# Kernel tuning notes

Measured on AMD Instinct MI355X. Metric: run time of the kernel, lower is better.

## Reference

```python
import jax, jax.numpy as jnp
import numpy as np
from jax.scipy.special import logsumexp

N = 4096
TAU = 2.0
IT = 30


def setup_inputs() -> dict:
    key = jax.random.key(0)
    k1, k2 = jax.random.split(key)
    eps = jax.random.normal(k1, (N, N), dtype=jnp.float32)
    mean = jax.random.uniform(k2, (N, N), dtype=jnp.float32)
    std = 10.0 * jnp.ones((N, N), dtype=jnp.float32)  # matches nn.Parameter(10*ones)
    return {"eps": eps, "mean": mean, "std": std}


def reference(eps, mean, std):
    # P_noisy = mean + std * eps ; Sinkhorn-Knopp in log domain, then exp.
    A = (mean + std * eps) / TAU

    def step(A, _):
        A = A - logsumexp(A, axis=1, keepdims=True)  # row normalize (log domain)
        A = A - logsumexp(A, axis=0, keepdims=True)  # col normalize (log domain)
        return A, None

    A, _ = jax.lax.scan(step, A, None, length=IT)
    return jnp.exp(A)
```

## Files before the change

kernel.cpp:

```cpp
#include <hip/hip_runtime.h>


constexpr int N    = 4096;
constexpr int IT   = 30;
constexpr int NBLK = 256;
constexpr int ROWS = 16;
constexpr int TPB  = 512;

typedef __attribute__((ext_vector_type(8))) unsigned short ushort8v;

__device__ inline float bf2f(unsigned int h) {
    union { unsigned int u; float f; } x; x.u = h << 16; return x.f;
}
__device__ inline unsigned short f2bf(float f) {
    union { float f; unsigned int u; } x; x.f = f;
    unsigned int r = x.u + 0x7FFFu + ((x.u >> 16) & 1u);
    return (unsigned short)(r >> 16);
}

struct V8 { float v[8]; };
struct V4 { float v[4]; };

template<typename PT> struct StoreOf;
template<> struct StoreOf<unsigned short> { using T = ushort8v; };
template<> struct StoreOf<float>          { using T = V8;       };

__device__ inline V8 unpackP(const ushort8v& s) {
    V8 r;
    #pragma unroll
    for (int k = 0; k < 8; ++k) r.v[k] = bf2f((unsigned int)s[k]);
    return r;
}
__device__ inline V8 unpackP(const V8& s) { return s; }

typedef __attribute__((ext_vector_type(4))) unsigned short ushort4v;
template<typename PT>
__device__ inline V4 loadP4(const PT* base, size_t e);
template<> __device__ inline V4 loadP4<unsigned short>(const unsigned short* base, size_t e) {
    ushort4v p = *(const ushort4v*)(base + e);
    V4 r;
    #pragma unroll
    for (int k = 0; k < 4; ++k) r.v[k] = bf2f((unsigned int)p[k]);
    return r;
}
template<> __device__ inline V4 loadP4<float>(const float* base, size_t e) {
    float4 a = *(const float4*)(base + e);
    V4 r = {{a.x, a.y, a.z, a.w}};
    return r;
}

template<typename PT>
__global__ __launch_bounds__(TPB) void k_first(const float* __restrict__ eps,
                                               const float* __restrict__ mean,
                                               const float* __restrict__ stdv,
                                               PT* __restrict__ P,
                                               float* __restrict__ partial,
                                               float* __restrict__ u_glob) {
    __shared__ float ldsRow[ROWS][8];
    __shared__ float ldsU[ROWS];
    const int t    = threadIdx.x;
    const int wv   = t >> 6, lane = t & 63;
    const int b    = blockIdx.x;
    const int col0 = t * 8;
    const int q    = t * 4;
    const int row0 = b * ROWS;

    typename StoreOf<PT>::T raw[ROWS];

    #pragma unroll
    for (int i = 0; i < ROWS; ++i) {
        const size_t rb = (size_t)(row0 + i) * N + col0;
        float4 e0 = *(const float4*)&eps [rb], e1 = *(const float4*)&eps [rb + 4];
        float4 m0 = *(const float4*)&mean[rb], m1 = *(const float4*)&mean[rb + 4];
        float4 s0 = *(const float4*)&stdv[rb], s1 = *(const float4*)&stdv[rb + 4];
        float p[8];
        p[0] = __expf((m0.x + s0.x * e0.x) * 0.5f);
        p[1] = __expf((m0.y + s0.y * e0.y) * 0.5f);
        p[2] = __expf((m0.z + s0.z * e0.z) * 0.5f);
        p[3] = __expf((m0.w + s0.w * e0.w) * 0.5f);
        p[4] = __expf((m1.x + s1.x * e1.x) * 0.5f);
        p[5] = __expf((m1.y + s1.y * e1.y) * 0.5f);
        p[6] = __expf((m1.z + s1.z * e1.z) * 0.5f);
        p[7] = __expf((m1.w + s1.w * e1.w) * 0.5f);
        if constexpr (sizeof(PT) == 2) {
            ushort8v o;
            #pragma unroll
            for (int k = 0; k < 8; ++k) o[k] = f2bf(p[k]);
            raw[i] = o;
            *(ushort8v*)((unsigned short*)P + rb) = o;
        } else {
            V8 r = {{p[0], p[1], p[2], p[3], p[4], p[5], p[6], p[7]}};
            raw[i] = r;
            float4 a = {p[0], p[1], p[2], p[3]}, bb = {p[4], p[5], p[6], p[7]};
            *(float4*)((float*)P + rb)     = a;
            *(float4*)((float*)P + rb + 4) = bb;
        }
    }

    #pragma unroll
    for (int i = 0; i < ROWS; ++i) {
        V8 pf = unpackP(raw[i]);
        float s = pf.v[0] + pf.v[1] + pf.v[2] + pf.v[3]
                + pf.v[4] + pf.v[5] + pf.v[6] + pf.v[7];
        #pragma unroll
        for (int off = 32; off; off >>= 1) s += __shfl_xor(s, off, 64);
        if (lane == 0) ldsRow[i][wv] = s;
    }
    __syncthreads();

    if (t < 8 * ROWS) {
        const int row = t >> 3, w = t & 7;
        float s = ldsRow[row][w];
        s += __shfl_xor(s, 1, 64);
        s += __shfl_xor(s, 2, 64);
        s += __shfl_xor(s, 4, 64);
        if (w == 0) {
            float u = __builtin_amdgcn_rcpf(s);
            ldsU[row] = u;
            u_glob[row0 + row] = u;
        }
    }
    __syncthreads();

    float acc[8] = {0, 0, 0, 0, 0, 0, 0, 0};
    #pragma unroll
    for (int i = 0; i < ROWS; ++i) {
        const float u = ldsU[i];
        V8 pf = unpackP(raw[i]);
        #pragma unroll
        for (int k = 0; k < 8; ++k) acc[k] += u * pf.v[k];
    }
    float4 a  = {acc[0], acc[1], acc[2], acc[3]};
    float4 bb = {acc[4], acc[5], acc[6], acc[7]};
    *(float4*)&partial[(size_t)b * N + q]        = a;
    *(float4*)&partial[(size_t)b * N + 2048 + q] = bb;
}

template<typename PT>
__global__ __launch_bounds__(TPB) void k_iter(const PT* __restrict__ P,
                                              const float* __restrict__ csum_prev,
                                              float* __restrict__ partial,
                                              float* __restrict__ u_glob) {
    __shared__ float ldsRow[ROWS][8];
    __shared__ float ldsU[ROWS];
    const int t    = threadIdx.x;
    const int wv   = t >> 6, lane = t & 63;
    const int b    = blockIdx.x;
    const int col0 = t * 8;
    const int q    = t * 4;
    const int row0 = b * ROWS;

    float4 c0 = *(const float4*)&csum_prev[q];
    float4 c1 = *(const float4*)&csum_prev[2048 + q];
    float v[8];
    v[0] = __builtin_amdgcn_rcpf(c0.x);  v[1] = __builtin_amdgcn_rcpf(c0.y);
    v[2] = __builtin_amdgcn_rcpf(c0.z);  v[3] = __builtin_amdgcn_rcpf(c0.w);
    v[4] = __builtin_amdgcn_rcpf(c1.x);  v[5] = __builtin_amdgcn_rcpf(c1.y);
    v[6] = __builtin_amdgcn_rcpf(c1.z);  v[7] = __builtin_amdgcn_rcpf(c1.w);

    typename StoreOf<PT>::T raw[ROWS];
    #pragma unroll
    for (int i = 0; i < ROWS; ++i)
        raw[i] = *(const typename StoreOf<PT>::T*)(P + (size_t)(row0 + i) * N + col0);

    #pragma unroll
    for (int i = 0; i < ROWS; ++i) {
        V8 pf = unpackP(raw[i]);
        float s = pf.v[0] * v[0] + pf.v[1] * v[1] + pf.v[2] * v[2] + pf.v[3] * v[3]
                + pf.v[4] * v[4] + pf.v[5] * v[5] + pf.v[6] * v[6] + pf.v[7] * v[7];
        #pragma unroll
        for (int off = 32; off; off >>= 1) s += __shfl_xor(s, off, 64);
        if (lane == 0) ldsRow[i][wv] = s;
    }
    __syncthreads();

    if (t < 8 * ROWS) {
        const int row = t >> 3, w = t & 7;
        float s = ldsRow[row][w];
        s += __shfl_xor(s, 1, 64);
        s += __shfl_xor(s, 2, 64);
        s += __shfl_xor(s, 4, 64);
        if (w == 0) {
            float u = __builtin_amdgcn_rcpf(s);
            ldsU[row] = u;
            u_glob[row0 + row] = u;
        }
    }
    __syncthreads();

    float acc[8] = {0, 0, 0, 0, 0, 0, 0, 0};
    #pragma unroll
    for (int i = 0; i < ROWS; ++i) {
        const float u = ldsU[i];
        V8 pf = unpackP(raw[i]);
        #pragma unroll
        for (int k = 0; k < 8; ++k) acc[k] += u * pf.v[k];
    }
    float4 a  = {acc[0], acc[1], acc[2], acc[3]};
    float4 bb = {acc[4], acc[5], acc[6], acc[7]};
    *(float4*)&partial[(size_t)b * N + q]        = a;
    *(float4*)&partial[(size_t)b * N + 2048 + q] = bb;
}

__global__ __launch_bounds__(512) void k_reduce(const float* __restrict__ partial,
                                                float* __restrict__ csum_cur) {
    __shared__ float red[16][32];
    const int t = threadIdx.x;
    const int lane = t & 63, wv = t >> 6;
    const int c     = blockIdx.x * 32 + (lane & 31);
    const int slice = wv * 2 + (lane >> 5);
    const float* p = partial + (size_t)(slice * 16) * N + c;
    float s = 0.0f;
    #pragma unroll 16
    for (int r = 0; r < 16; ++r)
        s += p[(size_t)r * N];
    red[slice][lane & 31] = s;
    __syncthreads();
    if (t < 32) {
        float acc = 0.0f;
        #pragma unroll
        for (int sl = 0; sl < 16; ++sl) acc += red[sl][t];
        csum_cur[blockIdx.x * 32 + t] = acc;
    }
}

template<typename PT>
__global__ __launch_bounds__(256) void k_final(const PT* __restrict__ P,
                                               const float* __restrict__ u_glob,
                                               const float* __restrict__ csum_last,
                                               float* __restrict__ out) {
    const int idx = blockIdx.x * 256 + threadIdx.x;
    const int row = idx >> 10;
    const int c4  = (idx & 1023) * 4;
    const float u = u_glob[row];
    const int perm = ((c4 & 4) ? 2048 : 0) + ((c4 >> 3) << 2);
    float4 cc = *(const float4*)&csum_last[perm];
    V4 p = loadP4(P, (size_t)row * N + c4);
    float4 r;
    r.x = p.v[0] * u * __builtin_amdgcn_rcpf(cc.x);
    r.y = p.v[1] * u * __builtin_amdgcn_rcpf(cc.y);
    r.z = p.v[2] * u * __builtin_amdgcn_rcpf(cc.z);
    r.w = p.v[3] * u * __builtin_amdgcn_rcpf(cc.w);
    ((float4*)out)[(size_t)idx] = r;
}

extern "C" void kernel_launch(void* const* d_in, const int* in_sizes, int n_in,
                              void* d_out, int out_size, void* d_ws, size_t ws_size,
                              hipStream_t stream) {
    const float* eps  = (const float*)d_in[0];
    const float* mean = (const float*)d_in[1];
    const float* stdv = (const float*)d_in[2];
    float* out = (float*)d_out;
    char* ws = (char*)d_ws;

    float* bufA   = (float*)ws;
    float* bufB   = bufA + N;
    float* u_glob = bufB + N;
    const size_t partOff = 64 * 1024;
    float* partial = (float*)(ws + partOff);
    const size_t partBytes = (size_t)NBLK * N * sizeof(float);
    const size_t pOff   = partOff + partBytes;
    const size_t pBytes = (size_t)N * N * sizeof(unsigned short);

    const int finalGrid = N * N / 4 / 256;

    float* cs[2] = { bufA, bufB };

    if (ws_size >= pOff + pBytes) {
        unsigned short* P = (unsigned short*)(ws + pOff);
        k_first<unsigned short><<<NBLK, TPB, 0, stream>>>(eps, mean, stdv, P, partial, u_glob);
        k_reduce<<<128, 512, 0, stream>>>(partial, cs[1]);
        for (int t = 2; t <= IT; ++t) {
            k_iter<unsigned short><<<NBLK, TPB, 0, stream>>>(P, cs[(t - 1) & 1], partial, u_glob);
            k_reduce<<<128, 512, 0, stream>>>(partial, cs[t & 1]);
        }
        k_final<unsigned short><<<finalGrid, 256, 0, stream>>>(P, u_glob, cs[IT & 1], out);
    } else {
        float* P = out;
        k_first<float><<<NBLK, TPB, 0, stream>>>(eps, mean, stdv, P, partial, u_glob);
        k_reduce<<<128, 512, 0, stream>>>(partial, cs[1]);
        for (int t = 2; t <= IT; ++t) {
            k_iter<float><<<NBLK, TPB, 0, stream>>>(P, cs[(t - 1) & 1], partial, u_glob);
            k_reduce<<<128, 512, 0, stream>>>(partial, cs[t & 1]);
        }
        k_final<float><<<finalGrid, 256, 0, stream>>>(P, u_glob, cs[IT & 1], out);
    }
}
```

Baseline: 586.2 us.

## Fuse Sinkhorn iterations into persistent kernel with register-resident P and grid barriers

Replaces the roughly sixty per-iteration kernel launches with one persistent kernel of 256 blocks. Each block keeps its 16-row slice of P in registers as bf16 for all iterations, so P is never re-read from global memory. Blocks sync through an atomic grid barrier, the column reduction is spread across blocks, and the final scaling is done in place. This removes launch overhead and the repeated P reads, but it relies on all 256 blocks being co-resident and adds two grid barriers per iteration.

```diff
diff --git a/kernel.cpp b/kernel.cpp
--- a/kernel.cpp
+++ b/kernel.cpp
@@ -21,52 +21,195 @@
 struct V8 { float v[8]; };
 struct V4 { float v[4]; };
 
-template<typename PT> struct StoreOf;
-template<> struct StoreOf<unsigned short> { using T = ushort8v; };
-template<> struct StoreOf<float>          { using T = V8;       };
-
-__device__ inline V8 unpackP(const ushort8v& s) {
+__device__ inline V8 unpack8(const ushort8v& s) {
     V8 r;
     #pragma unroll
     for (int k = 0; k < 8; ++k) r.v[k] = bf2f((unsigned int)s[k]);
     return r;
 }
-__device__ inline V8 unpackP(const V8& s) { return s; }
-
-typedef __attribute__((ext_vector_type(4))) unsigned short ushort4v;
-template<typename PT>
-__device__ inline V4 loadP4(const PT* base, size_t e);
-template<> __device__ inline V4 loadP4<unsigned short>(const unsigned short* base, size_t e) {
-    ushort4v p = *(const ushort4v*)(base + e);
-    V4 r;
-    #pragma unroll
-    for (int k = 0; k < 4; ++k) r.v[k] = bf2f((unsigned int)p[k]);
-    return r;
-}
-template<> __device__ inline V4 loadP4<float>(const float* base, size_t e) {
+
+__device__ inline void gbar(unsigned* bar, unsigned target) {
+    __syncthreads();
+    if (threadIdx.x == 0) {
+        __builtin_amdgcn_fence(__ATOMIC_RELEASE, "agent");
+        __hip_atomic_fetch_add(bar, 1u, __ATOMIC_RELAXED, __HIP_MEMORY_SCOPE_AGENT);
+        while (__hip_atomic_load(bar, __ATOMIC_RELAXED,
+                                 __HIP_MEMORY_SCOPE_AGENT) < target)
+            __builtin_amdgcn_s_sleep(1);
+        __builtin_amdgcn_fence(__ATOMIC_ACQUIRE, "agent");
+    }
+    __syncthreads();
+}
+
+__global__ __launch_bounds__(TPB, 2) void k_persist(
+        const float* __restrict__ eps, const float* __restrict__ mean,
+        const float* __restrict__ stdv, float* __restrict__ out,
+        float* __restrict__ partial, float* __restrict__ csum,
+        unsigned* __restrict__ bar) {
+    __shared__ float ldsRow[ROWS][8];
+    __shared__ float ldsU[ROWS];
+    __shared__ float red[32][16];
+    const int t = threadIdx.x, wv = t >> 6, lane = t & 63;
+    const int b = blockIdx.x;
+    const int col0 = t * 8;
+    const int row0 = b * ROWS;
+    unsigned bcnt = 0;
+
+    ushort8v P[ROWS];
+    #pragma unroll
+    for (int i = 0; i < ROWS; ++i) {
+        const size_t rb = (size_t)(row0 + i) * N + col0;
+        float4 e0 = *(const float4*)&eps [rb], e1 = *(const float4*)&eps [rb + 4];
+        float4 m0 = *(const float4*)&mean[rb], m1 = *(const float4*)&mean[rb + 4];
+        float4 s0 = *(const float4*)&stdv[rb], s1 = *(const float4*)&stdv[rb + 4];
+        ushort8v o;
+        o[0] = f2bf(__expf((m0.x + s0.x * e0.x) * 0.5f));
+        o[1] = f2bf(__expf((m0.y + s0.y * e0.y) * 0.5f));
+        o[2] = f2bf(__expf((m0.z + s0.z * e0.z) * 0.5f));
+        o[3] = f2bf(__expf((m0.w + s0.w * e0.w) * 0.5f));
+        o[4] = f2bf(__expf((m1.x + s1.x * e1.x) * 0.5f));
+        o[5] = f2bf(__expf((m1.y + s1.y * e1.y) * 0.5f));
+        o[6] = f2bf(__expf((m1.z + s1.z * e1.z) * 0.5f));
+        o[7] = f2bf(__expf((m1.w + s1.w * e1.w) * 0.5f));
+        P[i] = o;
+    }
+
+    #pragma unroll
+    for (int i = 0; i < ROWS; ++i) {
+        V8 pf = unpack8(P[i]);
+        float s = pf.v[0] + pf.v[1] + pf.v[2] + pf.v[3]
+                + pf.v[4] + pf.v[5] + pf.v[6] + pf.v[7];
+        #pragma unroll
+        for (int off = 32; off; off >>= 1) s += __shfl_xor(s, off, 64);
+        if (lane == 0) ldsRow[i][wv] = s;
+    }
+    __syncthreads();
+    if (t < 8 * ROWS) {
+        const int row = t >> 3, w = t & 7;
+        float s = ldsRow[row][w];
+        s += __shfl_xor(s, 1, 64);
+        s += __shfl_xor(s, 2, 64);
+        s += __shfl_xor(s, 4, 64);
+        if (w == 0) ldsU[row] = __builtin_amdgcn_rcpf(s);
+    }
+    __syncthreads();
+    {
+        float acc[8] = {0, 0, 0, 0, 0, 0, 0, 0};
+        #pragma unroll
+        for (int i = 0; i < ROWS; ++i) {
+            const float u = ldsU[i];
+            V8 pf = unpack8(P[i]);
+            #pragma unroll
+            for (int k = 0; k < 8; ++k) acc[k] += u * pf.v[k];
+        }
+        float4 a  = {acc[0], acc[1], acc[2], acc[3]};
+        float4 bb = {acc[4], acc[5], acc[6], acc[7]};
+        *(float4*)&partial[(size_t)b * N + col0]     = a;
+        *(float4*)&partial[(size_t)b * N + col0 + 4] = bb;
+    }
+
+    for (int it = 1; ; ++it) {
+        gbar(bar, (++bcnt) * NBLK);
+        {
+            const int col = row0 + (t & 15);
+            const int ch  = t >> 4;
+            const float* pp = partial + (size_t)(ch * 8) * N + col;
+            float s = 0.0f;
+            #pragma unroll
+            for (int r = 0; r < 8; ++r) s += pp[(size_t)r * N];
+            red[ch][t & 15] = s;
+        }
+        __syncthreads();
+        if (t < 16) {
+            float a = 0.0f;
+            #pragma unroll
+            for (int c = 0; c < 32; ++c) a += red[c][t];
+            csum[row0 + t] = a;
+        }
+        gbar(bar, (++bcnt) * NBLK);
+        if (it == IT) break;
+
+        float4 c0 = *(const float4*)&csum[col0];
+        float4 c1 = *(const float4*)&csum[col0 + 4];
+        float v[8];
+        v[0] = __builtin_amdgcn_rcpf(c0.x);  v[1] = __builtin_amdgcn_rcpf(c0.y);
+        v[2] = __builtin_amdgcn_rcpf(c0.z);  v[3] = __builtin_amdgcn_rcpf(c0.w);
+        v[4] = __builtin_amdgcn_rcpf(c1.x);  v[5] = __builtin_amdgcn_rcpf(c1.y);
+        v[6] = __builtin_amdgcn_rcpf(c1.z);  v[7] = __builtin_amdgcn_rcpf(c1.w);
+
+        #pragma unroll
+        for (int i = 0; i < ROWS; ++i) {
+            V8 pf = unpack8(P[i]);
+            float s = pf.v[0] * v[0] + pf.v[1] * v[1] + pf.v[2] * v[2] + pf.v[3] * v[3]
+                    + pf.v[4] * v[4] + pf.v[5] * v[5] + pf.v[6] * v[6] + pf.v[7] * v[7];
+            #pragma unroll
+            for (int off = 32; off; off >>= 1) s += __shfl_xor(s, off, 64);
+            if (lane == 0) ldsRow[i][wv] = s;
+        }
+        __syncthreads();
+        if (t < 8 * ROWS) {
+            const int row = t >> 3, w = t & 7;
+            float s = ldsRow[row][w];
+            s += __shfl_xor(s, 1, 64);
+            s += __shfl_xor(s, 2, 64);
+            s += __shfl_xor(s, 4, 64);
+            if (w == 0) ldsU[row] = __builtin_amdgcn_rcpf(s);
+        }
+        __syncthreads();
+        float acc[8] = {0, 0, 0, 0, 0, 0, 0, 0};
+        #pragma unroll
+        for (int i = 0; i < ROWS; ++i) {
+            const float u = ldsU[i];
+            V8 pf = unpack8(P[i]);
+            #pragma unroll
+            for (int k = 0; k < 8; ++k) acc[k] += u * pf.v[k];
+        }
+        float4 a  = {acc[0], acc[1], acc[2], acc[3]};
+        float4 bb = {acc[4], acc[5], acc[6], acc[7]};
+        *(float4*)&partial[(size_t)b * N + col0]     = a;
+        *(float4*)&partial[(size_t)b * N + col0 + 4] = bb;
+    }
+
+    float4 c0 = *(const float4*)&csum[col0];
+    float4 c1 = *(const float4*)&csum[col0 + 4];
+    float v[8];
+    v[0] = __builtin_amdgcn_rcpf(c0.x);  v[1] = __builtin_amdgcn_rcpf(c0.y);
+    v[2] = __builtin_amdgcn_rcpf(c0.z);  v[3] = __builtin_amdgcn_rcpf(c0.w);
+    v[4] = __builtin_amdgcn_rcpf(c1.x);  v[5] = __builtin_amdgcn_rcpf(c1.y);
+    v[6] = __builtin_amdgcn_rcpf(c1.z);  v[7] = __builtin_amdgcn_rcpf(c1.w);
+    #pragma unroll
+    for (int i = 0; i < ROWS; ++i) {
+        const float u = ldsU[i];
+        V8 pf = unpack8(P[i]);
+        float4 a  = {pf.v[0] * u * v[0], pf.v[1] * u * v[1],
+                     pf.v[2] * u * v[2], pf.v[3] * u * v[3]};
+        float4 bb = {pf.v[4] * u * v[4], pf.v[5] * u * v[5],
+                     pf.v[6] * u * v[6], pf.v[7] * u * v[7]};
+        const size_t rb = (size_t)(row0 + i) * N + col0;
+        *(float4*)&out[rb]     = a;
+        *(float4*)&out[rb + 4] = bb;
+    }
+}
+
+__device__ inline V4 loadP4f(const float* base, size_t e) {
     float4 a = *(const float4*)(base + e);
     V4 r = {{a.x, a.y, a.z, a.w}};
     return r;
 }
 
-template<typename PT>
-__global__ __launch_bounds__(TPB) void k_first(const float* __restrict__ eps,
-                                               const float* __restrict__ mean,
-                                               const float* __restrict__ stdv,
-                                               PT* __restrict__ P,
-                                               float* __restrict__ partial,
-                                               float* __restrict__ u_glob) {
+__global__ __launch_bounds__(TPB) void k_first_f(const float* __restrict__ eps,
+                                                 const float* __restrict__ mean,
+                                                 const float* __restrict__ stdv,
+                                                 float* __restrict__ P,
+                                                 float* __restrict__ partial,
+                                                 float* __restrict__ u_glob) {
     __shared__ float ldsRow[ROWS][8];
     __shared__ float ldsU[ROWS];
-    const int t    = threadIdx.x;
-    const int wv   = t >> 6, lane = t & 63;
-    const int b    = blockIdx.x;
-    const int col0 = t * 8;
-    const int q    = t * 4;
-    const int row0 = b * ROWS;
-
-    typename StoreOf<PT>::T raw[ROWS];
-
+    const int t = threadIdx.x, wv = t >> 6, lane = t & 63;
+    const int b = blockIdx.x;
+    const int col0 = t * 8, q = t * 4, row0 = b * ROWS;
+
+    V8 raw[ROWS];
     #pragma unroll
     for (int i = 0; i < ROWS; ++i) {
         const size_t rb = (size_t)(row0 + i) * N + col0;
@@ -82,32 +225,21 @@
         p[5] = __expf((m1.y + s1.y * e1.y) * 0.5f);
         p[6] = __expf((m1.z + s1.z * e1.z) * 0.5f);
         p[7] = __expf((m1.w + s1.w * e1.w) * 0.5f);
-        if constexpr (sizeof(PT) == 2) {
-            ushort8v o;
-            #pragma unroll
-            for (int k = 0; k < 8; ++k) o[k] = f2bf(p[k]);
-            raw[i] = o;
-            *(ushort8v*)((unsigned short*)P + rb) = o;
-        } else {
-            V8 r = {{p[0], p[1], p[2], p[3], p[4], p[5], p[6], p[7]}};
-            raw[i] = r;
-            float4 a = {p[0], p[1], p[2], p[3]}, bb = {p[4], p[5], p[6], p[7]};
-            *(float4*)((float*)P + rb)     = a;
-            *(float4*)((float*)P + rb + 4) = bb;
-        }
-    }
-
-    #pragma unroll
-    for (int i = 0; i < ROWS; ++i) {
-        V8 pf = unpackP(raw[i]);
-        float s = pf.v[0] + pf.v[1] + pf.v[2] + pf.v[3]
-                + pf.v[4] + pf.v[5] + pf.v[6] + pf.v[7];
+        V8 r = {{p[0], p[1], p[2], p[3], p[4], p[5], p[6], p[7]}};
+        raw[i] = r;
+        float4 a = {p[0], p[1], p[2], p[3]}, bb = {p[4], p[5], p[6], p[7]};
+        *(float4*)(P + rb)     = a;
+        *(float4*)(P + rb + 4) = bb;
+    }
+    #pragma unroll
+    for (int i = 0; i < ROWS; ++i) {
+        float s = raw[i].v[0] + raw[i].v[1] + raw[i].v[2] + raw[i].v[3]
+                + raw[i].v[4] + raw[i].v[5] + raw[i].v[6] + raw[i].v[7];
         #pragma unroll
         for (int off = 32; off; off >>= 1) s += __shfl_xor(s, off, 64);
         if (lane == 0) ldsRow[i][wv] = s;
     }
     __syncthreads();
-
     if (t < 8 * ROWS) {
         const int row = t >> 3, w = t & 7;
         float s = ldsRow[row][w];
@@ -121,14 +253,12 @@
         }
     }
     __syncthreads();
-
     float acc[8] = {0, 0, 0, 0, 0, 0, 0, 0};
     #pragma unroll
     for (int i = 0; i < ROWS; ++i) {
         const float u = ldsU[i];
-        V8 pf = unpackP(raw[i]);
-        #pragma unroll
-        for (int k = 0; k < 8; ++k) acc[k] += u * pf.v[k];
+        #pragma unroll
+        for (int k = 0; k < 8; ++k) acc[k] += u * raw[i].v[k];
     }
     float4 a  = {acc[0], acc[1], acc[2], acc[3]};
     float4 bb = {acc[4], acc[5], acc[6], acc[7]};
@@ -136,19 +266,15 @@
     *(float4*)&partial[(size_t)b * N + 2048 + q] = bb;
 }
 
-template<typename PT>
-__global__ __launch_bounds__(TPB) void k_iter(const PT* __restrict__ P,
-                                              const float* __restrict__ csum_prev,
-                                              float* __restrict__ partial,
-                                              float* __restrict__ u_glob) {
+__global__ __launch_bounds__(TPB) void k_iter_f(const float* __restrict__ P,
+                                                const float* __restrict__ csum_prev,
+                                                float* __restrict__ partial,
+                                                float* __restrict__ u_glob) {
     __shared__ float ldsRow[ROWS][8];
     __shared__ float ldsU[ROWS];
-    const int t    = threadIdx.x;
-    const int wv   = t >> 6, lane = t & 63;
-    const int b    = blockIdx.x;
-    const int col0 = t * 8;
-    const int q    = t * 4;
-    const int row0 = b * ROWS;
+    const int t = threadIdx.x, wv = t >> 6, lane = t & 63;
+    const int b = blockIdx.x;
+    const int col0 = t * 8, q = t * 4, row0 = b * ROWS;
 
     float4 c0 = *(const float4*)&csum_prev[q];
     float4 c1 = *(const float4*)&csum_prev[2048 + q];
@@ -158,22 +284,24 @@
     v[4] = __builtin_amdgcn_rcpf(c1.x);  v[5] = __builtin_amdgcn_rcpf(c1.y);
     v[6] = __builtin_amdgcn_rcpf(c1.z);  v[7] = __builtin_amdgcn_rcpf(c1.w);
 
-    typename StoreOf<PT>::T raw[ROWS];
-    #pragma unroll
-    for (int i = 0; i < ROWS; ++i)
-        raw[i] = *(const typename StoreOf<PT>::T*)(P + (size_t)(row0 + i) * N + col0);
-
-    #pragma unroll
-    for (int i = 0; i < ROWS; ++i) {
-        V8 pf = unpackP(raw[i]);
-        float s = pf.v[0] * v[0] + pf.v[1] * v[1] + pf.v[2] * v[2] + pf.v[3] * v[3]
-                + pf.v[4] * v[4] + pf.v[5] * v[5] + pf.v[6] * v[6] + pf.v[7] * v[7];
+    V8 raw[ROWS];
+    #pragma unroll
+    for (int i = 0; i < ROWS; ++i) {
+        const size_t rb = (size_t)(row0 + i) * N + col0;
+        float4 a = *(const float4*)(P + rb);
+        float4 bb = *(const float4*)(P + rb + 4);
+        V8 r = {{a.x, a.y, a.z, a.w, bb.x, bb.y, bb.z, bb.w}};
+        raw[i] = r;
+    }
+    #pragma unroll
+    for (int i = 0; i < ROWS; ++i) {
+        float s = raw[i].v[0] * v[0] + raw[i].v[1] * v[1] + raw[i].v[2] * v[2] + raw[i].v[3] * v[3]
+                + raw[i].v[4] * v[4] + raw[i].v[5] * v[5] + raw[i].v[6] * v[6] + raw[i].v[7] * v[7];
         #pragma unroll
         for (int off = 32; off; off >>= 1) s += __shfl_xor(s, off, 64);
         if (lane == 0) ldsRow[i][wv] = s;
     }
     __syncthreads();
-
     if (t < 8 * ROWS) {
         const int row = t >> 3, w = t & 7;
         float s = ldsRow[row][w];
@@ -187,14 +315,12 @@
         }
     }
     __syncthreads();
-
     float acc[8] = {0, 0, 0, 0, 0, 0, 0, 0};
     #pragma unroll
     for (int i = 0; i < ROWS; ++i) {
         const float u = ldsU[i];
-        V8 pf = unpackP(raw[i]);
-        #pragma unroll
-        for (int k = 0; k < 8; ++k) acc[k] += u * pf.v[k];
+        #pragma unroll
+        for (int k = 0; k < 8; ++k) acc[k] += u * raw[i].v[k];
     }
     float4 a  = {acc[0], acc[1], acc[2], acc[3]};
     float4 bb = {acc[4], acc[5], acc[6], acc[7]};
@@ -224,18 +350,17 @@
     }
 }
 
-template<typename PT>
-__global__ __launch_bounds__(256) void k_final(const PT* __restrict__ P,
-                                               const float* __restrict__ u_glob,
-                                               const float* __restrict__ csum_last,
-                                               float* __restrict__ out) {
+__global__ __launch_bounds__(256) void k_final_f(const float* __restrict__ P,
+                                                 const float* __restrict__ u_glob,
+                                                 const float* __restrict__ csum_last,
+                                                 float* __restrict__ out) {
     const int idx = blockIdx.x * 256 + threadIdx.x;
     const int row = idx >> 10;
     const int c4  = (idx & 1023) * 4;
     const float u = u_glob[row];
     const int perm = ((c4 & 4) ? 2048 : 0) + ((c4 >> 3) << 2);
     float4 cc = *(const float4*)&csum_last[perm];
-    V4 p = loadP4(P, (size_t)row * N + c4);
+    V4 p = loadP4f(P, (size_t)row * N + c4);
     float4 r;
     r.x = p.v[0] * u * __builtin_amdgcn_rcpf(cc.x);
     r.y = p.v[1] * u * __builtin_amdgcn_rcpf(cc.y);
@@ -256,33 +381,27 @@
     float* bufA   = (float*)ws;
     float* bufB   = bufA + N;
     float* u_glob = bufB + N;
+    unsigned* bar = (unsigned*)(ws + 48 * 1024);
     const size_t partOff = 64 * 1024;
     float* partial = (float*)(ws + partOff);
     const size_t partBytes = (size_t)NBLK * N * sizeof(float);
-    const size_t pOff   = partOff + partBytes;
-    const size_t pBytes = (size_t)N * N * sizeof(unsigned short);
+
+    if (ws_size >= partOff + partBytes) {
+        float* csum = bufA;
+        hipMemsetAsync(bar, 0, sizeof(unsigned), stream);
+        k_persist<<<dim3(NBLK), dim3(TPB), 0, stream>>>(
+            eps, mean, stdv, out, partial, csum, bar);
+        return;
+    }
 
     const int finalGrid = N * N / 4 / 256;
-
     float* cs[2] = { bufA, bufB };
-
-    if (ws_size >= pOff + pBytes) {
-        unsigned short* P = (unsigned short*)(ws + pOff);
-        k_first<unsigned short><<<NBLK, TPB, 0, stream>>>(eps, mean, stdv, P, partial, u_glob);
-        k_reduce<<<128, 512, 0, stream>>>(partial, cs[1]);
-        for (int t = 2; t <= IT; ++t) {
-            k_iter<unsigned short><<<NBLK, TPB, 0, stream>>>(P, cs[(t - 1) & 1], partial, u_glob);
-            k_reduce<<<128, 512, 0, stream>>>(partial, cs[t & 1]);
-        }
-        k_final<unsigned short><<<finalGrid, 256, 0, stream>>>(P, u_glob, cs[IT & 1], out);
-    } else {
-        float* P = out;
-        k_first<float><<<NBLK, TPB, 0, stream>>>(eps, mean, stdv, P, partial, u_glob);
-        k_reduce<<<128, 512, 0, stream>>>(partial, cs[1]);
-        for (int t = 2; t <= IT; ++t) {
-            k_iter<float><<<NBLK, TPB, 0, stream>>>(P, cs[(t - 1) & 1], partial, u_glob);
-            k_reduce<<<128, 512, 0, stream>>>(partial, cs[t & 1]);
-        }
-        k_final<float><<<finalGrid, 256, 0, stream>>>(P, u_glob, cs[IT & 1], out);
-    }
-}
+    float* P = out;
+    k_first_f<<<NBLK, TPB, 0, stream>>>(eps, mean, stdv, P, partial, u_glob);
+    k_reduce<<<128, 512, 0, stream>>>(partial, cs[1]);
+    for (int t = 2; t <= IT; ++t) {
+        k_iter_f<<<NBLK, TPB, 0, stream>>>(P, cs[(t - 1) & 1], partial, u_glob);
+        k_reduce<<<128, 512, 0, stream>>>(partial, cs[t & 1]);
+    }
+    k_final_f<<<finalGrid, 256, 0, stream>>>(P, u_glob, cs[IT & 1], out);
+}
```

New measurement: 1.883 ms. 221% more time.
